# Optimization experiments

Hardware: AMD Instinct MI355X
Metric: run time of the kernel (lower is better)

The kernel has to match this reference:

```python
import jax, jax.numpy as jnp
import numpy as np

B, S, D, H = 2, 2048, 1024, 16
DK = D // H  # 64
ROPE_BASE = 10000.0


def _rope_tables(dk, seq_len, base=ROPE_BASE):
    inv_freq = 1.0 / base ** (jnp.arange(0, dk, 2, dtype=jnp.float32) / dk)
    t = jnp.arange(seq_len, dtype=jnp.float32)
    freqs = t[:, None] * inv_freq[None, :]            # [S, dk/2]
    cos = jnp.repeat(jnp.cos(freqs), 2, axis=-1)      # [S, dk] (repeat_interleave)
    sin = jnp.repeat(jnp.sin(freqs), 2, axis=-1)
    return cos, sin


def _rotate_half(x):
    x1, x2 = jnp.split(x, 2, axis=-1)
    return jnp.concatenate((-x2, x1), axis=-1)


def setup_inputs() -> dict:
    key = jax.random.key(0)
    ks = jax.random.split(key, 9)
    scale = 0.02
    x = jax.random.normal(ks[0], (B, S, D), jnp.float32)
    wq = jax.random.normal(ks[1], (D, D), jnp.float32) * scale
    wk = jax.random.normal(ks[2], (D, D), jnp.float32) * scale
    wv = jax.random.normal(ks[3], (D, D), jnp.float32) * scale
    wo = jax.random.normal(ks[4], (D, D), jnp.float32) * scale
    bq = jnp.zeros((D,), jnp.float32)
    bk = jnp.zeros((D,), jnp.float32)
    bv = jnp.zeros((D,), jnp.float32)
    bo = jnp.zeros((D,), jnp.float32)
    mask = jnp.tril(jnp.ones((S, S), dtype=bool))[None, None]  # [1,1,S,S] causal
    return {"x": x, "mask": mask, "wq": wq, "bq": bq, "wk": wk, "bk": bk,
            "wv": wv, "bv": bv, "wo": wo, "bo": bo}


def reference(x, mask, wq, bq, wk, bk, wv, bv, wo, bo):
    b, s, d = x.shape
    h, dk = H, DK
    # QKV projections (nn.Linear: x @ W^T + b), split heads -> [B,H,S,dk]
    q = (x @ wq.T + bq).reshape(b, s, h, dk).transpose(0, 2, 1, 3)
    k = (x @ wk.T + bk).reshape(b, s, h, dk).transpose(0, 2, 1, 3)
    v = (x @ wv.T + bv).reshape(b, s, h, dk).transpose(0, 2, 1, 3)
    # RoPE
    cos, sin = _rope_tables(dk, s)                    # [S, dk]
    cos = cos[None, None]                             # [1,1,S,dk]
    sin = sin[None, None]
    q = q * cos + _rotate_half(q) * sin
    k = k * cos + _rotate_half(k) * sin
    # Naive attention: full [B,H,S,S] scores
    scores = jnp.einsum("bhqd,bhkd->bhqk", q, k) / np.float32(np.sqrt(dk))
    scores = jnp.where(mask, scores, jnp.float32(-1e9))
    attn = jax.nn.softmax(scores, axis=-1)
    out = jnp.einsum("bhqk,bhkd->bhqd", attn, v)      # [B,H,S,dk]
    out = out.transpose(0, 2, 1, 3).reshape(b, s, d)  # [B,S,D]
    return out @ wo.T + bo
```

## Files before the change

### kernel.cpp

```cpp
#include <hip/hip_runtime.h>
#include <hip/hip_bf16.h>

#define B_ 2
#define S_ 2048
#define D_ 1024
#define H_ 16
#define DK_ 64
#define BH_ (B_*H_)

typedef __attribute__((ext_vector_type(8))) short short8;
typedef __attribute__((ext_vector_type(4))) short short4v;
typedef __attribute__((ext_vector_type(4))) float f32x4;

__device__ __forceinline__ unsigned short f2bf(float f) {
  unsigned u = __float_as_uint(f);
  u += 0x7FFFu + ((u >> 16) & 1u);
  return (unsigned short)(u >> 16);
}
__device__ __forceinline__ float bf2f(unsigned short b) {
  return __uint_as_float(((unsigned)b) << 16);
}
__device__ __forceinline__ unsigned pk2bf(float lo, float hi) {
  float2 f; f.x = lo; f.y = hi;
  __hip_bfloat162 t = __float22bfloat162_rn(f);
  unsigned r; __builtin_memcpy(&r, &t, 4); return r;
}
__device__ __forceinline__ float fexp2(float x) {
  float r; asm("v_exp_f32 %0, %1" : "=v"(r) : "v"(x)); return r;
}

__device__ __forceinline__ long ftile_off(int n, int k, int ktiles) {
  return ((long)(n >> 7) * ktiles + (k >> 5)) * 4096 + ((k >> 3) & 3) * 1024 + (n & 127) * 8 + (k & 7);
}

__global__ __launch_bounds__(256) void cvt_kernel(const float* __restrict__ x, const float* __restrict__ wq,
                           const float* __restrict__ wk, const float* __restrict__ wv,
                           const float* __restrict__ wo, const float* __restrict__ bq,
                           const float* __restrict__ bk, const float* __restrict__ bv,
                           unsigned short* __restrict__ xb, unsigned short* __restrict__ wqkvb,
                           unsigned short* __restrict__ wob, float* __restrict__ bqkv) {
  const int bi = blockIdx.x;
  if (bi >= 2048) {
    const int i = (bi - 2048) * 1024 + (int)threadIdx.x * 4;
    const float* bb = (i < D_) ? (bq + i) : ((i < 2 * D_) ? (bk + i - D_) : (bv + i - 2 * D_));
    *(float4*)(bqkv + i) = *(const float4*)bb;
    return;
  }
  __shared__ alignas(16) unsigned short lt[4096];
  const int t = threadIdx.x;
  const int r = t >> 1, kb = (t & 1) * 16;
  int ti; unsigned short* dst;
  if (bi < 1024) { ti = bi; dst = xb; }
  else if (bi < 1792) { ti = bi - 1024; dst = wqkvb; }
  else { ti = bi - 1792; dst = wob; }
  const int rt = ti >> 5, kt = ti & 31;
  const int grow = rt * 128 + r;
  const float* sp;
  if (bi < 1024) sp = x + (long)grow * 1024 + kt * 32 + kb;
  else if (bi < 1792) {
    const float* w = (grow < 1024) ? wq : ((grow < 2048) ? wk : wv);
    sp = w + (long)(grow & 1023) * 1024 + kt * 32 + kb;
  } else sp = wo + (long)grow * 1024 + kt * 32 + kb;

  const float4 va = ((const float4*)sp)[0], vb = ((const float4*)sp)[1];
  const float4 vc = ((const float4*)sp)[2], vd = ((const float4*)sp)[3];
  short8 o0, o1;
  o0[0] = f2bf(va.x); o0[1] = f2bf(va.y); o0[2] = f2bf(va.z); o0[3] = f2bf(va.w);
  o0[4] = f2bf(vb.x); o0[5] = f2bf(vb.y); o0[6] = f2bf(vb.z); o0[7] = f2bf(vb.w);
  o1[0] = f2bf(vc.x); o1[1] = f2bf(vc.y); o1[2] = f2bf(vc.z); o1[3] = f2bf(vc.w);
  o1[4] = f2bf(vd.x); o1[5] = f2bf(vd.y); o1[6] = f2bf(vd.z); o1[7] = f2bf(vd.w);
  const int kc0 = kb >> 3;
  *(short8*)(lt + kc0 * 1024 + r * 8) = o0;
  *(short8*)(lt + (kc0 + 1) * 1024 + r * 8) = o1;
  __syncthreads();
  unsigned short* dp = dst + ((long)rt * 32 + kt) * 4096 + t * 16;
  *(short8*)dp       = *(const short8*)(lt + t * 16);
  *(short8*)(dp + 8) = *(const short8*)(lt + t * 16 + 8);
}

template<bool OUT_F32>
__global__ __launch_bounds__(256) void gemm_bt(const unsigned short* __restrict__ A,
                                               const unsigned short* __restrict__ Bm,
                                               const float* __restrict__ bias,
                                               void* __restrict__ Cp, int M, int N, int K) {
  __shared__ alignas(16) unsigned short As[4096];
  __shared__ alignas(16) unsigned short Bs[4096];
  const int t = threadIdx.x;
  const int w = t >> 6;
  const int lane = t & 63;
  const int brow = blockIdx.y * 128;
  const int bcol = blockIdx.x * 128;
  const int wr = (w >> 1) * 64, wc = (w & 1) * 64;
  const int fr = lane & 15;
  const int g = lane >> 4;
  const int ktiles = K >> 5;
  f32x4 acc[4][4] = {};

  for (int kt = 0; kt < ktiles; ++kt) {
    const unsigned short* Asrc = A  + ((long)blockIdx.y * ktiles + kt) * 4096;
    const unsigned short* Bsrc = Bm + ((long)blockIdx.x * ktiles + kt) * 4096;
#pragma unroll
    for (int j = 0; j < 2; ++j) {
      const int off = (w * 2 + j) * 512;
      __builtin_amdgcn_global_load_lds((const __attribute__((address_space(1))) void*)(Asrc + off + lane * 8),
                                       (__attribute__((address_space(3))) void*)(As + off), 16, 0, 0);
      __builtin_amdgcn_global_load_lds((const __attribute__((address_space(1))) void*)(Bsrc + off + lane * 8),
                                       (__attribute__((address_space(3))) void*)(Bs + off), 16, 0, 0);
    }
    __syncthreads();
    short8 a[4], b[4];
#pragma unroll
    for (int m = 0; m < 4; ++m)
      a[m] = *(const short8*)(As + g * 1024 + (wr + m * 16 + fr) * 8);
#pragma unroll
    for (int n = 0; n < 4; ++n)
      b[n] = *(const short8*)(Bs + g * 1024 + (wc + n * 16 + fr) * 8);
#pragma unroll
    for (int m = 0; m < 4; ++m)
#pragma unroll
      for (int n = 0; n < 4; ++n)
        acc[m][n] = __builtin_amdgcn_mfma_f32_16x16x32_bf16(a[m], b[n], acc[m][n], 0, 0, 0);
    __syncthreads();
  }

#pragma unroll
  for (int m = 0; m < 4; ++m) {
#pragma unroll
    for (int n = 0; n < 4; ++n) {
      const int col = bcol + wc + n * 16 + fr;
      const float bv_ = bias[col];
#pragma unroll
      for (int i = 0; i < 4; ++i) {
        const int row = brow + wr + m * 16 + g * 4 + i;
        const float v = acc[m][n][i] + bv_;
        if (OUT_F32) ((float*)Cp)[(long)row * N + col] = v;
        else ((unsigned short*)Cp)[(long)row * N + col] = f2bf(v);
      }
    }
  }
}

__global__ void rope_kernel(const unsigned short* __restrict__ qkv,
                            unsigned short* __restrict__ Qh,
                            unsigned short* __restrict__ Kf) {
  const int idx = blockIdx.x * blockDim.x + threadIdx.x;
  const int d = idx & 63;
  const int s = (idx >> 6) & (S_ - 1);
  const int bh = idx >> 17;
  const int b = bh >> 4, h = bh & 15;
  const long qrow = (long)(b * S_ + s) * 3072 + h * 64;
  const float qv = bf2f(qkv[qrow + d]);
  const float kv = bf2f(qkv[qrow + 1024 + d]);
  const int dp = (d < 32) ? d + 32 : d - 32;
  const float qp = bf2f(qkv[qrow + dp]);
  const float kp = bf2f(qkv[qrow + 1024 + dp]);
  const int j = d >> 1;
  const float invf = __expf(-(float)j * 0.28782313662425574f);
  const float fr = (float)s * invf;
  float sn, cs;
  __sincosf(fr, &sn, &cs);
  const float qo = (d < 32) ? (qv * cs - qp * sn) : (qv * cs + qp * sn);
  const float ko = (d < 32) ? (kv * cs - kp * sn) : (kv * cs + kp * sn);
  Qh[(long)bh * S_ * DK_ + (long)s * DK_ + d] = f2bf(qo * 0.18033688011112043f);
  const long kfo = (long)bh * (S_ * DK_) + (long)(s >> 4) * 1024 +
                   (long)(d >> 5) * 512 + (long)((d >> 3) & 3) * 128 + (s & 15) * 8 + (d & 7);
  Kf[kfo] = f2bf(ko);
}

__global__ __launch_bounds__(256) void vtrans_kernel(const unsigned short* __restrict__ qkv,
                                                     unsigned short* __restrict__ Vf) {
  __shared__ unsigned short tile[32][72];
  const int bh = blockIdx.y;
  const int b = bh >> 4, h = bh & 15;
  const int c32 = blockIdx.x;
  const int tid = threadIdx.x;
  {
    const int r = tid >> 3, d0 = (tid & 7) * 8;
    *(short8*)&tile[r][d0] =
        *(const short8*)(qkv + (long)(b * S_ + c32 * 32 + r) * 3072 + 2048 + h * 64 + d0);
  }
  __syncthreads();
  const int t = tid >> 6, g = (tid >> 4) & 3, fr = tid & 15;
  short8 o;
#pragma unroll
  for (int j = 0; j < 8; ++j) {
    const int r = (j < 4) ? (4 * g + j) : (16 + 4 * g + (j - 4));
    o[j] = tile[r][t * 16 + fr];
  }
  *(short8*)(Vf + ((long)(bh * 64 + c32)) * 2048 + t * 512 + g * 128 + fr * 8) = o;
}

__global__ __launch_bounds__(256) void flash_kernel(const unsigned short* __restrict__ Qh,
                                                    const unsigned short* __restrict__ Kf,
                                                    const unsigned short* __restrict__ Vf,
                                                    unsigned short* __restrict__ attnout) {
  __shared__ alignas(16) unsigned short Ks[8192];
  __shared__ alignas(16) unsigned short Vs[8192];

  const int flat = (int)blockIdx.x;
  const int xcd = flat & 7;
  const int ix  = flat >> 3;
  const int k   = ix >> 5;
  const int c   = ix & 31;
  const int bh  = xcd * 4 + k;
  const int qblk = (k & 1) ? c : 31 - c;

  const int b = bh >> 4, h = bh & 15;
  const int w = threadIdx.x >> 6, lane = threadIdx.x & 63;
  const int fr = lane & 15, g = lane >> 4;
  const int qg = qblk * 64 + w * 16 + fr;

  const unsigned short* Qb = Qh + (long)bh * (S_ * DK_);
  const short8 qf0 = *(const short8*)(Qb + (long)qg * DK_ + g * 8);
  const short8 qf1 = *(const short8*)(Qb + (long)qg * DK_ + 32 + g * 8);

  short8 vone;
#pragma unroll
  for (int i = 0; i < 8; ++i) vone[i] = (short)0x3F80;

  f32x4 acc[4] = {};
  f32x4 acl = {};

  const unsigned short* kfb = Kf + (long)bh * (S_ * DK_);
  const unsigned short* vfb = Vf + (long)bh * (S_ * DK_);
  const int kvend = qblk * 64;
  const int frag = g * 128 + fr * 8;

  for (int kv0 = 0; kv0 <= kvend; kv0 += 128) {
    {
      const unsigned short* gk = kfb + (long)kv0 * 64 + w * 2048 + lane * 8;
      unsigned short* lk = Ks + w * 2048;
      const unsigned short* gv = vfb + (long)kv0 * 64 + w * 2048 + lane * 8;
      unsigned short* lv = Vs + w * 2048;
#pragma unroll
      for (int cc = 0; cc < 4; ++cc) {
        __builtin_amdgcn_global_load_lds((const __attribute__((address_space(1))) void*)(gk + cc * 512),
                                         (__attribute__((address_space(3))) void*)(lk + cc * 512), 16, 0, 0);
        __builtin_amdgcn_global_load_lds((const __attribute__((address_space(1))) void*)(gv + cc * 512),
                                         (__attribute__((address_space(3))) void*)(lv + cc * 512), 16, 0, 0);
      }
    }
    __syncthreads();
    const bool domask = (kv0 + 128 > kvend);

#pragma unroll
    for (int sub = 0; sub < 2; ++sub) {
      const unsigned short* ksb = Ks + sub * 4096;
      const unsigned short* vsb = Vs + sub * 4096;

      f32x4 st[4];
      __builtin_amdgcn_s_setprio(1);
#pragma unroll
      for (int cc = 0; cc < 4; ++cc) {
        const short8 k0 = *(const short8*)(ksb + cc * 1024 + frag);
        const short8 k1 = *(const short8*)(ksb + cc * 1024 + 512 + frag);
        f32x4 z = {};
        z = __builtin_amdgcn_mfma_f32_16x16x32_bf16(k0, qf0, z, 0, 0, 0);
        z = __builtin_amdgcn_mfma_f32_16x16x32_bf16(k1, qf1, z, 0, 0, 0);
        st[cc] = z;
      }
      __builtin_amdgcn_s_setprio(0);

      if (domask) {
        const int base = kv0 + sub * 64 + g * 4;
#pragma unroll
        for (int cc = 0; cc < 4; ++cc)
#pragma unroll
          for (int i = 0; i < 4; ++i)
            if (base + cc * 16 + i > qg) st[cc][i] = -3.0e38f;
      }

      float ps[16];
#pragma unroll
      for (int cc = 0; cc < 4; ++cc)
#pragma unroll
        for (int i = 0; i < 4; ++i) ps[cc * 4 + i] = fexp2(st[cc][i]);

      union { short8 s8; unsigned u[4]; } P0, P1;
#pragma unroll
      for (int i = 0; i < 4; ++i) {
        P0.u[i] = pk2bf(ps[2 * i], ps[2 * i + 1]);
        P1.u[i] = pk2bf(ps[8 + 2 * i], ps[8 + 2 * i + 1]);
      }

      __builtin_amdgcn_s_setprio(1);
#pragma unroll
      for (int t = 0; t < 4; ++t) {
        const short8 va = *(const short8*)(vsb + t * 512 + frag);
        const short8 vb = *(const short8*)(vsb + 2048 + t * 512 + frag);
        acc[t] = __builtin_amdgcn_mfma_f32_16x16x32_bf16(va, P0.s8, acc[t], 0, 0, 0);
        acc[t] = __builtin_amdgcn_mfma_f32_16x16x32_bf16(vb, P1.s8, acc[t], 0, 0, 0);
      }
      acl = __builtin_amdgcn_mfma_f32_16x16x32_bf16(vone, P0.s8, acl, 0, 0, 0);
      acl = __builtin_amdgcn_mfma_f32_16x16x32_bf16(vone, P1.s8, acl, 0, 0, 0);
      __builtin_amdgcn_s_setprio(0);
    }
    __syncthreads();
  }

  const float ri = 1.0f / acl[0];
  const int row = b * S_ + qg;
#pragma unroll
  for (int t = 0; t < 4; ++t) {
    short4v ov;
#pragma unroll
    for (int i = 0; i < 4; ++i) ov[i] = (short)f2bf(acc[t][i] * ri);
    const int kcol = h * 64 + t * 16 + g * 4;
    *(short4v*)(attnout + ftile_off(row, kcol, 32)) = ov;
  }
}

extern "C" void kernel_launch(void* const* d_in, const int* in_sizes, int n_in,
                              void* d_out, int out_size, void* d_ws, size_t ws_size,
                              hipStream_t stream) {
  const float* x  = (const float*)d_in[0];
  const float* wq = (const float*)d_in[2];
  const float* bq = (const float*)d_in[3];
  const float* wk = (const float*)d_in[4];
  const float* bk = (const float*)d_in[5];
  const float* wv = (const float*)d_in[6];
  const float* bv = (const float*)d_in[7];
  const float* wo = (const float*)d_in[8];
  const float* bo = (const float*)d_in[9];

  const long NX = (long)B_ * S_ * D_;
  const long NW = (long)D_ * D_;

  unsigned short* xb    = (unsigned short*)d_ws;
  unsigned short* wqkvb = xb + NX;
  unsigned short* wob   = wqkvb + 3 * NW;
  float*          bqkv  = (float*)(wob + NW);
  unsigned short* qkv   = (unsigned short*)(bqkv + 3 * D_);
  unsigned short* Qh    = qkv + (long)(B_ * S_) * 3 * D_;
  unsigned short* Kf    = Qh + NX;
  unsigned short* Vf    = Kf + NX;
  unsigned short* attnout = xb;

  cvt_kernel<<<2051, 256, 0, stream>>>(x, wq, wk, wv, wo, bq, bk, bv,
                                       xb, wqkvb, wob, bqkv);
  gemm_bt<false><<<dim3(24, 32), 256, 0, stream>>>(xb, wqkvb, bqkv, qkv, 4096, 3072, 1024);
  rope_kernel<<<(int)(NX / 256), 256, 0, stream>>>(qkv, Qh, Kf);
  vtrans_kernel<<<dim3(64, BH_), 256, 0, stream>>>(qkv, Vf);
  flash_kernel<<<1024, 256, 0, stream>>>(Qh, Kf, Vf, attnout);
  gemm_bt<true><<<dim3(8, 32), 256, 0, stream>>>(attnout, wob, bo, d_out, 4096, 1024, 1024);
}
```

Measured before the change: 122.1 us.

## Fuse RoPE and V transpose into the QKV projection GEMM epilogue

Adds a dedicated QKV GEMM kernel whose epilogue applies the bias, RoPE rotation and Q scaling, then writes Q, K and V straight into the head-split and tiled layouts the flash kernel expects. This removes the separate rope and V-transpose kernels and the intermediate bf16 qkv buffer round trip, which saves two launches and one full write plus read of the qkv tensor. The catch is that the epilogue now does scattered 2-byte stores and computes sincos per element inside the GEMM, which could lengthen the GEMM tail.

Measured after the change: 118.8 us. -2.7%, faster.

```diff
diff --git a/kernel.cpp b/kernel.cpp
--- a/kernel.cpp
+++ b/kernel.cpp
@@ -31,6 +31,17 @@
 
 __device__ __forceinline__ long ftile_off(int n, int k, int ktiles) {
   return ((long)(n >> 7) * ktiles + (k >> 5)) * 4096 + ((k >> 3) & 3) * 1024 + (n & 127) * 8 + (k & 7);
+}
+
+__device__ __forceinline__ long kf_off(int bh, int s, int d) {
+  return (long)bh * (S_ * DK_) + (long)(s >> 4) * 1024 + (long)(d >> 5) * 512 +
+         (long)((d >> 3) & 3) * 128 + (s & 15) * 8 + (d & 7);
+}
+__device__ __forceinline__ long vf_off(int bh, int kv, int d) {
+  const int r = kv & 31;
+  const int g = (r & 15) >> 2;
+  const int j = (r < 16) ? (r & 3) : (4 + (r & 3));
+  return ((long)(bh * 64 + (kv >> 5))) * 2048 + (long)(d >> 4) * 512 + g * 128 + (d & 15) * 8 + j;
 }
 
 __global__ __launch_bounds__(256) void cvt_kernel(const float* __restrict__ x, const float* __restrict__ wq,
@@ -76,6 +87,111 @@
   unsigned short* dp = dst + ((long)rt * 32 + kt) * 4096 + t * 16;
   *(short8*)dp       = *(const short8*)(lt + t * 16);
   *(short8*)(dp + 8) = *(const short8*)(lt + t * 16 + 8);
+}
+
+__global__ __launch_bounds__(256) void gemm_qkv(const unsigned short* __restrict__ A,
+                                                const unsigned short* __restrict__ Bm,
+                                                const float* __restrict__ bias,
+                                                unsigned short* __restrict__ Qh,
+                                                unsigned short* __restrict__ Kf,
+                                                unsigned short* __restrict__ Vf) {
+  __shared__ alignas(16) unsigned short As[4096];
+  __shared__ alignas(16) unsigned short Bs[4096];
+  const int t = threadIdx.x;
+  const int w = t >> 6;
+  const int lane = t & 63;
+  const int bcol = blockIdx.x * 128;
+  const int wr = (w >> 1) * 64, wc = (w & 1) * 64;
+  const int fr = lane & 15;
+  const int g = lane >> 4;
+  const int ktiles = 32;
+  f32x4 acc[4][4] = {};
+
+  for (int kt = 0; kt < ktiles; ++kt) {
+    const unsigned short* Asrc = A  + ((long)blockIdx.y * ktiles + kt) * 4096;
+    const unsigned short* Bsrc = Bm + ((long)blockIdx.x * ktiles + kt) * 4096;
+#pragma unroll
+    for (int j = 0; j < 2; ++j) {
+      const int off = (w * 2 + j) * 512;
+      __builtin_amdgcn_global_load_lds((const __attribute__((address_space(1))) void*)(Asrc + off + lane * 8),
+                                       (__attribute__((address_space(3))) void*)(As + off), 16, 0, 0);
+      __builtin_amdgcn_global_load_lds((const __attribute__((address_space(1))) void*)(Bsrc + off + lane * 8),
+                                       (__attribute__((address_space(3))) void*)(Bs + off), 16, 0, 0);
+    }
+    __syncthreads();
+    short8 a[4], b[4];
+#pragma unroll
+    for (int m = 0; m < 4; ++m)
+      a[m] = *(const short8*)(As + g * 1024 + (wr + m * 16 + fr) * 8);
+#pragma unroll
+    for (int n = 0; n < 4; ++n)
+      b[n] = *(const short8*)(Bs + g * 1024 + (wc + n * 16 + fr) * 8);
+#pragma unroll
+    for (int m = 0; m < 4; ++m)
+#pragma unroll
+      for (int n = 0; n < 4; ++n)
+        acc[m][n] = __builtin_amdgcn_mfma_f32_16x16x32_bf16(a[m], b[n], acc[m][n], 0, 0, 0);
+    __syncthreads();
+  }
+
+  const int colbase = bcol + wc;
+  const int ct = colbase >> 6;
+  if (ct < 32) {
+    const bool isQ = (ct < 16);
+    const int h = ct & 15;
+    const float QS = 0.18033688011112043f;
+#pragma unroll
+    for (int np = 0; np < 2; ++np) {
+      const int d1 = np * 16 + fr;
+      const int d2 = d1 + 32;
+      const float invf1 = fexp2((float)(d1 >> 1) * -0.4152410118609203f);
+      const float invf2 = fexp2((float)(d2 >> 1) * -0.4152410118609203f);
+      const float b1 = bias[colbase + np * 16 + fr];
+      const float b2 = bias[colbase + np * 16 + 32 + fr];
+#pragma unroll
+      for (int m = 0; m < 4; ++m) {
+#pragma unroll
+        for (int i = 0; i < 4; ++i) {
+          const int row = blockIdx.y * 128 + wr + m * 16 + g * 4 + i;
+          const int s = row & (S_ - 1);
+          const int bh = (row >> 11) * 16 + h;
+          float s1, c1, s2, c2;
+          __sincosf((float)s * invf1, &s1, &c1);
+          __sincosf((float)s * invf2, &s2, &c2);
+          const float v1 = acc[m][np][i] + b1;
+          const float v2 = acc[m][np + 2][i] + b2;
+          float o1 = v1 * c1 - v2 * s1;
+          float o2 = v2 * c2 + v1 * s2;
+          if (isQ) {
+            o1 *= QS; o2 *= QS;
+            unsigned short* qp = Qh + (long)bh * (S_ * DK_) + (long)s * DK_;
+            qp[d1] = f2bf(o1);
+            qp[d2] = f2bf(o2);
+          } else {
+            Kf[kf_off(bh, s, d1)] = f2bf(o1);
+            Kf[kf_off(bh, s, d2)] = f2bf(o2);
+          }
+        }
+      }
+    }
+  } else {
+    const int h = ct & 15;
+#pragma unroll
+    for (int n = 0; n < 4; ++n) {
+      const int d = n * 16 + fr;
+      const float bv_ = bias[colbase + n * 16 + fr];
+#pragma unroll
+      for (int m = 0; m < 4; ++m) {
+#pragma unroll
+        for (int i = 0; i < 4; ++i) {
+          const int row = blockIdx.y * 128 + wr + m * 16 + g * 4 + i;
+          const int s = row & (S_ - 1);
+          const int bh = (row >> 11) * 16 + h;
+          Vf[vf_off(bh, s, d)] = f2bf(acc[m][n][i] + bv_);
+        }
+      }
+    }
+  }
 }
 
 template<bool OUT_F32>
@@ -140,56 +256,6 @@
   }
 }
 
-__global__ void rope_kernel(const unsigned short* __restrict__ qkv,
-                            unsigned short* __restrict__ Qh,
-                            unsigned short* __restrict__ Kf) {
-  const int idx = blockIdx.x * blockDim.x + threadIdx.x;
-  const int d = idx & 63;
-  const int s = (idx >> 6) & (S_ - 1);
-  const int bh = idx >> 17;
-  const int b = bh >> 4, h = bh & 15;
-  const long qrow = (long)(b * S_ + s) * 3072 + h * 64;
-  const float qv = bf2f(qkv[qrow + d]);
-  const float kv = bf2f(qkv[qrow + 1024 + d]);
-  const int dp = (d < 32) ? d + 32 : d - 32;
-  const float qp = bf2f(qkv[qrow + dp]);
-  const float kp = bf2f(qkv[qrow + 1024 + dp]);
-  const int j = d >> 1;
-  const float invf = __expf(-(float)j * 0.28782313662425574f);
-  const float fr = (float)s * invf;
-  float sn, cs;
-  __sincosf(fr, &sn, &cs);
-  const float qo = (d < 32) ? (qv * cs - qp * sn) : (qv * cs + qp * sn);
-  const float ko = (d < 32) ? (kv * cs - kp * sn) : (kv * cs + kp * sn);
-  Qh[(long)bh * S_ * DK_ + (long)s * DK_ + d] = f2bf(qo * 0.18033688011112043f);
-  const long kfo = (long)bh * (S_ * DK_) + (long)(s >> 4) * 1024 +
-                   (long)(d >> 5) * 512 + (long)((d >> 3) & 3) * 128 + (s & 15) * 8 + (d & 7);
-  Kf[kfo] = f2bf(ko);
-}
-
-__global__ __launch_bounds__(256) void vtrans_kernel(const unsigned short* __restrict__ qkv,
-                                                     unsigned short* __restrict__ Vf) {
-  __shared__ unsigned short tile[32][72];
-  const int bh = blockIdx.y;
-  const int b = bh >> 4, h = bh & 15;
-  const int c32 = blockIdx.x;
-  const int tid = threadIdx.x;
-  {
-    const int r = tid >> 3, d0 = (tid & 7) * 8;
-    *(short8*)&tile[r][d0] =
-        *(const short8*)(qkv + (long)(b * S_ + c32 * 32 + r) * 3072 + 2048 + h * 64 + d0);
-  }
-  __syncthreads();
-  const int t = tid >> 6, g = (tid >> 4) & 3, fr = tid & 15;
-  short8 o;
-#pragma unroll
-  for (int j = 0; j < 8; ++j) {
-    const int r = (j < 4) ? (4 * g + j) : (16 + 4 * g + (j - 4));
-    o[j] = tile[r][t * 16 + fr];
-  }
-  *(short8*)(Vf + ((long)(bh * 64 + c32)) * 2048 + t * 512 + g * 128 + fr * 8) = o;
-}
-
 __global__ __launch_bounds__(256) void flash_kernel(const unsigned short* __restrict__ Qh,
                                                     const unsigned short* __restrict__ Kf,
                                                     const unsigned short* __restrict__ Vf,
@@ -330,17 +396,14 @@
   unsigned short* wqkvb = xb + NX;
   unsigned short* wob   = wqkvb + 3 * NW;
   float*          bqkv  = (float*)(wob + NW);
-  unsigned short* qkv   = (unsigned short*)(bqkv + 3 * D_);
-  unsigned short* Qh    = qkv + (long)(B_ * S_) * 3 * D_;
+  unsigned short* Qh    = (unsigned short*)(bqkv + 3 * D_);
   unsigned short* Kf    = Qh + NX;
   unsigned short* Vf    = Kf + NX;
   unsigned short* attnout = xb;
 
   cvt_kernel<<<2051, 256, 0, stream>>>(x, wq, wk, wv, wo, bq, bk, bv,
                                        xb, wqkvb, wob, bqkv);
-  gemm_bt<false><<<dim3(24, 32), 256, 0, stream>>>(xb, wqkvb, bqkv, qkv, 4096, 3072, 1024);
-  rope_kernel<<<(int)(NX / 256), 256, 0, stream>>>(qkv, Qh, Kf);
-  vtrans_kernel<<<dim3(64, BH_), 256, 0, stream>>>(qkv, Vf);
+  gemm_qkv<<<dim3(24, 32), 256, 0, stream>>>(xb, wqkvb, bqkv, Qh, Kf, Vf);
   flash_kernel<<<1024, 256, 0, stream>>>(Qh, Kf, Vf, attnout);
   gemm_bt<true><<<dim3(8, 32), 256, 0, stream>>>(attnout, wob, bo, d_out, 4096, 1024, 1024);
 }
```
